# Optimization experiments

Hardware: AMD Instinct MI355X
Metric: run time of the kernel (lower is better)

The kernel has to match this reference:

```python
import jax, jax.numpy as jnp
import numpy as np

B, S, D = 4, 4096, 64   # batch, seq_len, input_size
H, HD = 4, 16           # num_heads, head_dim


def setup_inputs() -> dict:
    key = jax.random.key(0)
    ks = jax.random.split(key, 9)
    sd = 1.0 / np.sqrt(D)          # torch Linear default uniform(-1/sqrt(fan_in), ...)
    so = 1.0 / np.sqrt(H * HD)
    u = lambda k, shape, s: jax.random.uniform(k, shape, jnp.float32, -s, s)
    return {
        "x": jax.random.normal(ks[0], (B, S, D), jnp.float32),
        "Wq": u(ks[1], (H, D, HD), sd), "bq": u(ks[2], (H, HD), sd),
        "Wk": u(ks[3], (H, D, HD), sd), "bk": u(ks[4], (H, HD), sd),
        "Wv": u(ks[5], (H, D, HD), sd), "bv": u(ks[6], (H, HD), sd),
        "Wo": u(ks[7], (H * HD, D), so), "bo": u(ks[8], (D,), so),
    }


def reference(x, Wq, bq, Wk, bk, Wv, bv, Wo, bo):
    # Batched per-head projections (fuses the original per-head Linear loop)
    q = jnp.einsum('bsd,hde->bhse', x, Wq) + bq[None, :, None, :]
    k = jnp.einsum('bsd,hde->bhse', x, Wk) + bk[None, :, None, :]
    v = jnp.einsum('bsd,hde->bhse', x, Wv) + bv[None, :, None, :]
    # scores: [B, H, S(query), S(key)]
    scores = jnp.einsum('bhse,bhte->bhst', q, k) / np.sqrt(HD).astype(np.float32)
    # FAITHFUL quirk: torch Softmax(dim=1) on [B,S,S] normalizes over the QUERY axis
    w = jax.nn.softmax(scores, axis=2)
    attended = jnp.einsum('bhst,bhte->bhse', w, v)          # [B,H,S,HD]
    concat = attended.transpose(0, 2, 1, 3).reshape(B, S, H * HD)
    out = concat @ Wo + bo                                   # [B,S,D]
    # FAITHFUL quirk: final softmax over the sequence axis (dim=1)
    return jax.nn.softmax(out, axis=1)
```

## Files before the change

kernel.cpp:

```cpp
#include <hip/hip_runtime.h>
#include <hip/hip_bf16.h>


#define BB 4
#define SS 4096
#define DD 64
#define HH 4
#define HDD 16

typedef unsigned int u32;
typedef unsigned short u16;
typedef __attribute__((ext_vector_type(8))) short bfrag;
typedef __attribute__((ext_vector_type(4))) float floatx4;
typedef __attribute__((ext_vector_type(16))) float floatx16;
typedef __attribute__((ext_vector_type(2))) u32 u32x2;
typedef __attribute__((ext_vector_type(4))) u32 u32x4;

#define LOG2E 1.4426950408889634074f
#define QSCALE (LOG2E * 0.25f)

__device__ __forceinline__ float fexp2(float x) {
#if __has_builtin(__builtin_amdgcn_exp2f)
  return __builtin_amdgcn_exp2f(x);
#else
  float r; asm("v_exp_f32 %0, %1" : "=v"(r) : "v"(x)); return r;
#endif
}
__device__ __forceinline__ float frcp(float x) {
#if __has_builtin(__builtin_amdgcn_rcpf)
  return __builtin_amdgcn_rcpf(x);
#else
  float r; asm("v_rcp_f32 %0, %1" : "=v"(r) : "v"(x)); return r;
#endif
}

__device__ __forceinline__ u16 f2bf(float f) {
  u32 u = __builtin_bit_cast(u32, f);
  return (u16)((u + 0x7FFFu + ((u >> 16) & 1u)) >> 16);
}
__device__ __forceinline__ u32 pack_bf(float lo, float hi) {
#if __has_builtin(__builtin_amdgcn_perm)
  return __builtin_amdgcn_perm(__builtin_bit_cast(u32, hi),
                               __builtin_bit_cast(u32, lo), 0x07060302u);
#else
  u32 a = __builtin_bit_cast(u32, lo);
  u32 b = __builtin_bit_cast(u32, hi);
  return (a >> 16) | (b & 0xFFFF0000u);
#endif
}

__device__ __forceinline__ void gload_lds16(const u16* g, u16* l) {
  __builtin_amdgcn_global_load_lds(
      (const __attribute__((address_space(1))) void*)(g),
      (__attribute__((address_space(3))) void*)(l), 16, 0, 0);
}

__device__ __forceinline__ int tmap(int c) {
  int c5 = c & 31;
  return (c & ~31) + (c5 & 3) + ((c5 >> 2) & 1) * 8 + ((c5 >> 3) & 1) * 16
       + ((c5 >> 4) & 1) * 4;
}

__global__ __launch_bounds__(256) void k_proj(
    const float* __restrict__ x,
    const float* __restrict__ Wq, const float* __restrict__ bq,
    const float* __restrict__ Wk, const float* __restrict__ bk,
    const float* __restrict__ Wv, const float* __restrict__ bv,
    u16* __restrict__ qb, u16* __restrict__ kfl, float* __restrict__ vf)
{
  __shared__ float xs[16 * 64];
  const int tid = threadIdx.x;
  const int blk = blockIdx.x;
  const int b   = blk >> 8;
  const int s0  = (blk & 255) << 4;
  ((float4*)xs)[tid] = ((const float4*)(x + ((size_t)b * SS + s0) * DD))[tid];
  __syncthreads();

  const int col = tid & 63, h = col >> 4, e = col & 15;
  const int rg  = tid >> 6;
  float aq[4] = {0,0,0,0}, ak[4] = {0,0,0,0}, av[4] = {0,0,0,0};
  const int wofs = h * (DD * HDD) + e;
#pragma unroll 4
  for (int d = 0; d < DD; ++d) {
    float wq = Wq[wofs + d * HDD];
    float wk = Wk[wofs + d * HDD];
    float wv = Wv[wofs + d * HDD];
    const float* xr = xs + (rg * 4) * 64 + d;
#pragma unroll
    for (int r = 0; r < 4; ++r) {
      float xv = xr[r * 64];
      aq[r] += xv * wq; ak[r] += xv * wk; av[r] += xv * wv;
    }
  }
  const float bqv = bq[col], bkv = bk[col], bvv = bv[col];
  const int bh = b * HH + h;
  size_t base = ((size_t)bh * SS + (s0 + rg * 4)) * HDD + e;
#pragma unroll
  for (int r = 0; r < 4; ++r) {
    int t = s0 + rg * 4 + r;
    qb[base + r * HDD] = f2bf((aq[r] + bqv) * QSCALE);
    vf[base + r * HDD] = av[r] + bvv;
    size_t kidx = (((size_t)bh * 128 + (t >> 5)) * 64
                 + (e >> 3) * 32 + (t & 31)) * 8 + (e & 7);
    kfl[kidx] = f2bf(ak[r] + bkv);
  }
}

__global__ __launch_bounds__(512, 4) void k_csvp(
    const u16* __restrict__ qb, const u16* __restrict__ kfl,
    const float* __restrict__ vf, u16* __restrict__ vp)
{
  __shared__ float vstage[128 * 16];
  __shared__ float cpart[2][128];
  __shared__ float rcl[128];
  const int tid = threadIdx.x;
  const int lane = tid & 63, w = tid >> 6;
  const int l31 = lane & 31, hl = lane >> 5;
  const int bx = blockIdx.x;
  const int bh = blockIdx.y;
  const int shalf = w >> 2;
  const size_t base = (size_t)bh * (SS * HDD);

  {
    const float4* vsrc4 = (const float4*)(vf + ((size_t)bh * SS + bx * 128) * HDD);
    ((float4*)vstage)[tid] = vsrc4[tid];
  }

  const int g = bx * 4 + (w & 3);
  const bfrag kf = *(const bfrag*)(kfl + (((size_t)bh * 128 + g) * 64 + lane) * 8);
  const u16* qpc = qb + base + ((size_t)shalf * 2048 + l31) * HDD + hl * 8;
  const floatx16 z16 = {0.f};
  float c0 = 0.f, c1 = 0.f, c2 = 0.f, c3 = 0.f;

#define LQ(i) (*(const bfrag*)(qpc + (size_t)(i) * (32 * HDD)))
#define ACCUM(dv)                                   \
  do {                                              \
    _Pragma("unroll")                               \
    for (int j = 0; j < 4; ++j) {                   \
      c0 += fexp2((dv)[4 * j + 0]);                 \
      c1 += fexp2((dv)[4 * j + 1]);                 \
      c2 += fexp2((dv)[4 * j + 2]);                 \
      c3 += fexp2((dv)[4 * j + 3]);                 \
    }                                               \
  } while (0)
#define STEP(qr, ri)                                                        \
  do {                                                                      \
    floatx16 dB = __builtin_amdgcn_mfma_f32_32x32x16_bf16(qr, kf, z16, 0, 0, 0); \
    qr = LQ(ri);                                                            \
    ACCUM(dA);                                                              \
    dA = dB;                                                                \
  } while (0)

  bfrag q0 = LQ(0), q1 = LQ(1), q2v = LQ(2), q3 = LQ(3);
  floatx16 dA = __builtin_amdgcn_mfma_f32_32x32x16_bf16(q0, kf, z16, 0, 0, 0);
  q0 = LQ(4);
#pragma unroll 1
  for (int o = 0; o < 2; ++o) {
#pragma unroll
    for (int i = 0; i < 32; i += 4) {
      STEP(q1,  i + 5);
      STEP(q2v, i + 6);
      STEP(q3,  i + 7);
      STEP(q0,  i + 8);
    }
    qpc += 32 * 32 * HDD;
  }
#undef STEP
#undef LQ
#undef ACCUM

  float c = (c0 + c1) + (c2 + c3);
  c += __shfl_xor(c, 32, 64);
  if (hl == 0)
    cpart[shalf][(w & 3) * 32 + l31] = c;
  __syncthreads();
  if (tid < 128)
    rcl[tid] = frcp(cpart[0][tid] + cpart[1][tid]);
  __syncthreads();

  if (tid < 256) {
    const int e = tid >> 4;
    const int h0 = bx & 1;
    const int poff = h0 * 16 + (tid & 15);
    const int cc = poff ^ (e & 7);
    const int h128 = h0 * 128;
    u32 r[4];
#pragma unroll
    for (int jj = 0; jj < 4; ++jj) {
      int ta = tmap(cc * 8 + 2 * jj)     - h128;
      int tb = tmap(cc * 8 + 2 * jj + 1) - h128;
      u16 lo = f2bf(vstage[ta * 16 + e] * rcl[ta]);
      u16 hi = f2bf(vstage[tb * 16 + e] * rcl[tb]);
      r[jj] = (u32)lo | ((u32)hi << 16);
    }
    u16* outb = vp + ((size_t)bh * 16 + (bx >> 1)) * 4096;
    u32x4 vv = {r[0], r[1], r[2], r[3]};
    *(u32x4*)(outb + e * 256 + poff * 8) = vv;
  }
}

__global__ __launch_bounds__(256, 4) void k_attn(
    const u16* __restrict__ qb, const u16* __restrict__ kfl,
    const u16* __restrict__ vp, float* __restrict__ attp)
{
  __shared__ __align__(16) u16 vls[2][4096];
  const int tid  = threadIdx.x;
  const int lane = tid & 63, w = tid >> 6;
  const int l31 = lane & 31, hl = lane >> 5;
  const int bh = blockIdx.z, b = bh >> 2, h = bh & 3;
  const int tph = blockIdx.y;
  const int s0 = blockIdx.x * 128 + w * 32;
  const size_t base = (size_t)bh * (SS * HDD);

  const bfrag qf = *(const bfrag*)(qb + base + (size_t)(s0 + l31) * HDD + hl * 8);
  const floatx16 z16 = {0.f};
  floatx16 acc0 = {0.f}, acc1 = {0.f};

  const u16* vsrc = vp  + ((size_t)bh * 16  + tph * 8)  * 4096;
  const u16* ksrc = kfl + ((size_t)bh * 128 + tph * 64) * 512;
  const int eb = l31 & 7;

#define STAGE(ch, buf)                                                \
  do {                                                                \
    const u16* gv = vsrc + (ch) * 4096 + w * 1024 + lane * 8;         \
    u16* lv = &vls[buf][0] + w * 1024;                                \
    gload_lds16(gv, lv);                                              \
    gload_lds16(gv + 512, lv + 512);                                  \
  } while (0)

  STAGE(0, 0);
  bfrag kfr[4];
#pragma unroll
  for (int g = 0; g < 4; ++g)
    kfr[g] = *(const bfrag*)(ksrc + (size_t)g * 512 + lane * 8);
  floatx16 dA = __builtin_amdgcn_mfma_f32_32x32x16_bf16(kfr[0], qf, z16, 0, 0, 0);

  u32x4 efL = {0,0,0,0}, efH = {0,0,0,0};
  u32x4 afA0 = {0,0,0,0}, afA1 = {0,0,0,0};
  u32x4 pf0, pf1;

#pragma unroll 1
  for (int ch = 0; ch < 8; ++ch) {
    asm volatile("s_waitcnt vmcnt(8)" ::: "memory");
    __builtin_amdgcn_s_barrier();
    __builtin_amdgcn_sched_barrier(0);
    if (ch < 7) STAGE(ch + 1, (ch + 1) & 1);

    const u16* vrow = &vls[ch & 1][0] + (l31 & 15) * 256;
    {
      const int cc = hl * 2;
      pf0 = *(const u32x4*)(vrow + ((cc ^ eb) << 3));
      pf1 = *(const u32x4*)(vrow + (((cc + 1) ^ eb) << 3));
    }

#pragma unroll
    for (int it = 0; it < 8; ++it) {
      __builtin_amdgcn_s_setprio(1);
      floatx16 dB;
      if (it < 7)
        dB = __builtin_amdgcn_mfma_f32_32x32x16_bf16(kfr[(it + 1) & 3], qf, z16, 0, 0, 0);
      else
        dB = __builtin_amdgcn_mfma_f32_32x32x16_bf16(kfr[0], qf, z16, 0, 0, 0);
      if (it > 0 || ch > 0) {
        acc0 = __builtin_amdgcn_mfma_f32_32x32x16_bf16(
            __builtin_bit_cast(bfrag, afA0), __builtin_bit_cast(bfrag, efL), acc0, 0, 0, 0);
        acc1 = __builtin_amdgcn_mfma_f32_32x32x16_bf16(
            __builtin_bit_cast(bfrag, afA1), __builtin_bit_cast(bfrag, efH), acc1, 0, 0, 0);
      }
      __builtin_amdgcn_s_setprio(0);

      if (it < 4)
        kfr[it & 3] = *(const bfrag*)(ksrc + (size_t)(ch * 4096 + (it + 4) * 512) + lane * 8);
      else if (ch < 7)
        kfr[it & 3] = *(const bfrag*)(ksrc + (size_t)((ch + 1) * 4096 + (it - 4) * 512) + lane * 8);

      afA0 = pf0; afA1 = pf1;
      if (it < 7) {
        const int cc = (it + 1) * 4 + hl * 2;
        pf0 = *(const u32x4*)(vrow + ((cc ^ eb) << 3));
        pf1 = *(const u32x4*)(vrow + (((cc + 1) ^ eb) << 3));
      }

      u32 w0 = pack_bf(fexp2(dA[0]),  fexp2(dA[1]));
      u32 w1 = pack_bf(fexp2(dA[2]),  fexp2(dA[3]));
      u32 w2 = pack_bf(fexp2(dA[4]),  fexp2(dA[5]));
      u32 w3 = pack_bf(fexp2(dA[6]),  fexp2(dA[7]));
      u32 w4 = pack_bf(fexp2(dA[8]),  fexp2(dA[9]));
      u32 w5 = pack_bf(fexp2(dA[10]), fexp2(dA[11]));
      u32 w6 = pack_bf(fexp2(dA[12]), fexp2(dA[13]));
      u32 w7 = pack_bf(fexp2(dA[14]), fexp2(dA[15]));
      efL = (u32x4){w0, w1, w2, w3};
      efH = (u32x4){w4, w5, w6, w7};
      dA = dB;
    }
  }
#undef STAGE

  acc0 = __builtin_amdgcn_mfma_f32_32x32x16_bf16(
      __builtin_bit_cast(bfrag, afA0), __builtin_bit_cast(bfrag, efL), acc0, 0, 0, 0);
  acc1 = __builtin_amdgcn_mfma_f32_32x32x16_bf16(
      __builtin_bit_cast(bfrag, afA1), __builtin_bit_cast(bfrag, efH), acc1, 0, 0, 0);

  floatx16 acc = acc0 + acc1;
  float* ao = attp + (((size_t)tph * BB + b) * SS + s0 + l31) * (HH * HDD)
            + h * HDD + 4 * hl;
  float4 lo4 = {acc[0], acc[1], acc[2], acc[3]};
  float4 hi4 = {acc[4], acc[5], acc[6], acc[7]};
  *(float4*)ao       = lo4;
  *(float4*)(ao + 8) = hi4;
}

__global__ __launch_bounds__(256) void k_oproj(
    const float* __restrict__ att, const float* __restrict__ Wo,
    const float* __restrict__ bo, float* __restrict__ outp,
    float* __restrict__ part)
{
  __shared__ float wols[64 * 64];
  __shared__ float atts[8][128];
  __shared__ float red[4][64];
  const int tid = threadIdx.x;
  const int blk = blockIdx.x;
  const int b = blk >> 9, s0 = (blk & 511) << 3;
#pragma unroll
  for (int i = 0; i < 4; ++i)
    ((float4*)wols)[tid + 256 * i] = ((const float4*)Wo)[tid + 256 * i];
  {
    const int r = tid >> 5, q = tid & 31;
    const int half = q >> 4, j4 = (q & 15) << 2;
    const float4 v = *(const float4*)(
        att + (((size_t)half * BB + b) * SS + s0 + r) * 64 + j4);
    *(float4*)(&atts[r][half * 64 + j4]) = v;
  }
  __syncthreads();

  const int d = tid & 63, sg = tid >> 6;
  const float bov = bo[d];
  float es = 0.f;
#pragma unroll
  for (int r = 0; r < 2; ++r) {
    const int row = sg * 2 + r;
    float acc = bov;
#pragma unroll
    for (int c = 0; c < 64; ++c)
      acc += (atts[row][c] + atts[row][64 + c]) * wols[c * 64 + d];
    outp[((size_t)b * SS + s0 + row) * 64 + d] = acc;
    es += fexp2(acc * LOG2E);
  }
  red[sg][d] = es;
  __syncthreads();
  if (tid < 64)
    part[((size_t)b * 512 + (blk & 511)) * 64 + tid] =
        red[0][tid] + red[1][tid] + red[2][tid] + red[3][tid];
}

__global__ __launch_bounds__(256) void k_softmax(
    const float* __restrict__ outp, const float* __restrict__ part,
    float* __restrict__ out)
{
  __shared__ float red[4][64];
  __shared__ float rs[64];
  const int tid = threadIdx.x, d = tid & 63, sg = tid >> 6;
  const int st = blockIdx.x;
  const int b = blockIdx.y;
  {
    float e = 0.f;
    const float* pp = part + ((size_t)b * 512 + sg * 128) * 64 + d;
#pragma unroll 8
    for (int c = 0; c < 128; ++c) e += pp[c * 64];
    red[sg][d] = e;
  }
  __syncthreads();
  if (tid < 64)
    rs[tid] = frcp(red[0][tid] + red[1][tid] + red[2][tid] + red[3][tid]);
  __syncthreads();
  const float r = rs[d];
  const size_t rowbase = ((size_t)b * SS + st * 64 + sg * 16) * 64 + d;
#pragma unroll 4
  for (int i = 0; i < 16; ++i)
    out[rowbase + i * 64] = fexp2(outp[rowbase + i * 64] * LOG2E) * r;
}

extern "C" void kernel_launch(void* const* d_in, const int* in_sizes, int n_in,
                              void* d_out, int out_size, void* d_ws, size_t ws_size,
                              hipStream_t stream) {
  const float* x  = (const float*)d_in[0];
  const float* Wq = (const float*)d_in[1];
  const float* bq = (const float*)d_in[2];
  const float* Wk = (const float*)d_in[3];
  const float* bk = (const float*)d_in[4];
  const float* Wv = (const float*)d_in[5];
  const float* bv = (const float*)d_in[6];
  const float* Wo = (const float*)d_in[7];
  const float* bo = (const float*)d_in[8];

  char* ws = (char*)d_ws;
  constexpr size_t QB_OFF  = 0;
  constexpr size_t KF_OFF  = (size_t)2  << 20;
  constexpr size_t VF_OFF  = (size_t)4  << 20;
  constexpr size_t VP_OFF  = (size_t)8  << 20;
  constexpr size_t ATT_OFF = (size_t)10 << 20;
  constexpr size_t OUT_OFF = (size_t)18 << 20;
  constexpr size_t PT_OFF  = (size_t)22 << 20;

  u16*   qb   = (u16*)  (ws + QB_OFF);
  u16*   kfl  = (u16*)  (ws + KF_OFF);
  float* vf   = (float*)(ws + VF_OFF);
  u16*   vpb  = (u16*)  (ws + VP_OFF);
  float* attp = (float*)(ws + ATT_OFF);
  float* outp = (float*)(ws + OUT_OFF);
  float* part = (float*)(ws + PT_OFF);
  float* out  = (float*)d_out;

  hipLaunchKernelGGL(k_proj,    dim3(1024),       dim3(256), 0, stream,
                     x, Wq, bq, Wk, bk, Wv, bv, qb, kfl, vf);
  hipLaunchKernelGGL(k_csvp,    dim3(32, 16),     dim3(512), 0, stream,
                     qb, kfl, vf, vpb);
  hipLaunchKernelGGL(k_attn,    dim3(32, 2, 16),  dim3(256), 0, stream,
                     qb, kfl, vpb, attp);
  hipLaunchKernelGGL(k_oproj,   dim3(2048),       dim3(256), 0, stream,
                     attp, Wo, bo, outp, part);
  hipLaunchKernelGGL(k_softmax, dim3(64, 4),      dim3(256), 0, stream, outp, part, out);
}
```

Before: 181.0 us.

## Stage K tiles through double-buffered LDS alongside V instead of per-wave global loads

K fragments are now copied into a second double-buffered LDS array with the same async global-to-LDS path as V, once per block. Before, every wave read the identical K data directly from global memory into registers. The chunk loop is fully unrolled, waits for all outstanding loads at each barrier, and restarts the QK^T MFMA chain at the start of each chunk. This removes the cross-chunk score prefetch and the one-step-ahead V fragment prefetch. It cuts redundant global K traffic per block, at the cost of doubled LDS use, a pipeline bubble at each chunk boundary and a stricter wait.

```diff
diff --git a/kernel.cpp b/kernel.cpp
--- a/kernel.cpp
+++ b/kernel.cpp
@@ -204,6 +204,7 @@
     const u16* __restrict__ vp, float* __restrict__ attp)
 {
   __shared__ __align__(16) u16 vls[2][4096];
+  __shared__ __align__(16) u16 kls[2][4096];
   const int tid  = threadIdx.x;
   const int lane = tid & 63, w = tid >> 6;
   const int l31 = lane & 31, hl = lane >> 5;
@@ -226,59 +227,52 @@
     u16* lv = &vls[buf][0] + w * 1024;                                \
     gload_lds16(gv, lv);                                              \
     gload_lds16(gv + 512, lv + 512);                                  \
+    const u16* gk = ksrc + (ch) * 4096 + w * 1024 + lane * 8;         \
+    u16* lk = &kls[buf][0] + w * 1024;                                \
+    gload_lds16(gk, lk);                                              \
+    gload_lds16(gk + 512, lk + 512);                                  \
   } while (0)
 
   STAGE(0, 0);
-  bfrag kfr[4];
-#pragma unroll
-  for (int g = 0; g < 4; ++g)
-    kfr[g] = *(const bfrag*)(ksrc + (size_t)g * 512 + lane * 8);
-  floatx16 dA = __builtin_amdgcn_mfma_f32_32x32x16_bf16(kfr[0], qf, z16, 0, 0, 0);
 
   u32x4 efL = {0,0,0,0}, efH = {0,0,0,0};
-  u32x4 afA0 = {0,0,0,0}, afA1 = {0,0,0,0};
-  u32x4 pf0, pf1;
-
-#pragma unroll 1
+  u32x4 af0 = {0,0,0,0}, af1 = {0,0,0,0};
+
+#pragma unroll
   for (int ch = 0; ch < 8; ++ch) {
-    asm volatile("s_waitcnt vmcnt(8)" ::: "memory");
+    asm volatile("s_waitcnt vmcnt(0)" ::: "memory");
     __builtin_amdgcn_s_barrier();
     __builtin_amdgcn_sched_barrier(0);
     if (ch < 7) STAGE(ch + 1, (ch + 1) & 1);
 
     const u16* vrow = &vls[ch & 1][0] + (l31 & 15) * 256;
-    {
-      const int cc = hl * 2;
-      pf0 = *(const u32x4*)(vrow + ((cc ^ eb) << 3));
-      pf1 = *(const u32x4*)(vrow + (((cc + 1) ^ eb) << 3));
-    }
+    const u16* krow = &kls[ch & 1][0];
+
+    bfrag kc = *(const bfrag*)(krow + lane * 8);
+    floatx16 dA = __builtin_amdgcn_mfma_f32_32x32x16_bf16(kc, qf, z16, 0, 0, 0);
+    kc = *(const bfrag*)(krow + 512 + lane * 8);
 
 #pragma unroll
     for (int it = 0; it < 8; ++it) {
       __builtin_amdgcn_s_setprio(1);
       floatx16 dB;
       if (it < 7)
-        dB = __builtin_amdgcn_mfma_f32_32x32x16_bf16(kfr[(it + 1) & 3], qf, z16, 0, 0, 0);
-      else
-        dB = __builtin_amdgcn_mfma_f32_32x32x16_bf16(kfr[0], qf, z16, 0, 0, 0);
-      if (it > 0 || ch > 0) {
+        dB = __builtin_amdgcn_mfma_f32_32x32x16_bf16(kc, qf, z16, 0, 0, 0);
+      if (ch > 0 || it > 0) {
         acc0 = __builtin_amdgcn_mfma_f32_32x32x16_bf16(
-            __builtin_bit_cast(bfrag, afA0), __builtin_bit_cast(bfrag, efL), acc0, 0, 0, 0);
+            __builtin_bit_cast(bfrag, af0), __builtin_bit_cast(bfrag, efL), acc0, 0, 0, 0);
         acc1 = __builtin_amdgcn_mfma_f32_32x32x16_bf16(
-            __builtin_bit_cast(bfrag, afA1), __builtin_bit_cast(bfrag, efH), acc1, 0, 0, 0);
+            __builtin_bit_cast(bfrag, af1), __builtin_bit_cast(bfrag, efH), acc1, 0, 0, 0);
       }
       __builtin_amdgcn_s_setprio(0);
 
-      if (it < 4)
-        kfr[it & 3] = *(const bfrag*)(ksrc + (size_t)(ch * 4096 + (it + 4) * 512) + lane * 8);
-      else if (ch < 7)
-        kfr[it & 3] = *(const bfrag*)(ksrc + (size_t)((ch + 1) * 4096 + (it - 4) * 512) + lane * 8);
-
-      afA0 = pf0; afA1 = pf1;
-      if (it < 7) {
-        const int cc = (it + 1) * 4 + hl * 2;
-        pf0 = *(const u32x4*)(vrow + ((cc ^ eb) << 3));
-        pf1 = *(const u32x4*)(vrow + (((cc + 1) ^ eb) << 3));
+      if (it < 6)
+        kc = *(const bfrag*)(krow + (it + 2) * 512 + lane * 8);
+
+      {
+        const int cc = it * 4 + hl * 2;
+        af0 = *(const u32x4*)(vrow + ((cc ^ eb) << 3));
+        af1 = *(const u32x4*)(vrow + (((cc + 1) ^ eb) << 3));
       }
 
       u32 w0 = pack_bf(fexp2(dA[0]),  fexp2(dA[1]));
@@ -291,15 +285,15 @@
       u32 w7 = pack_bf(fexp2(dA[14]), fexp2(dA[15]));
       efL = (u32x4){w0, w1, w2, w3};
       efH = (u32x4){w4, w5, w6, w7};
-      dA = dB;
+      if (it < 7) dA = dB;
     }
   }
 #undef STAGE
 
   acc0 = __builtin_amdgcn_mfma_f32_32x32x16_bf16(
-      __builtin_bit_cast(bfrag, afA0), __builtin_bit_cast(bfrag, efL), acc0, 0, 0, 0);
+      __builtin_bit_cast(bfrag, af0), __builtin_bit_cast(bfrag, efL), acc0, 0, 0, 0);
   acc1 = __builtin_amdgcn_mfma_f32_32x32x16_bf16(
-      __builtin_bit_cast(bfrag, afA1), __builtin_bit_cast(bfrag, efH), acc1, 0, 0, 0);
+      __builtin_bit_cast(bfrag, af1), __builtin_bit_cast(bfrag, efH), acc1, 0, 0, 0);
 
   floatx16 acc = acc0 + acc1;
   float* ao = attp + (((size_t)tph * BB + b) * SS + s0 + l31) * (HH * HDD)
```

Measured after the change: 174.2 us, median of 2. 3.7% less time.
